# Performance work log

Measured on AMD Instinct MI355X. Metric: run time of the kernel, lower is better.

## Reference

```python
import jax, jax.numpy as jnp
import numpy as np

HEAD_DIM = 128
NUM_Q_HEADS = 16
NUM_KV_HEADS = 8
EPS = 1e-6


def _rope_tables(seq_len, head_dim, base=10000.0):
    inv_freq = 1.0 / (base ** (np.arange(0, head_dim, 2, dtype=np.float32) / head_dim))
    t = np.arange(seq_len, dtype=np.float32)
    freqs = np.outer(t, inv_freq)                      # [S, hd/2]
    emb = np.concatenate([freqs, freqs], axis=-1)      # [S, hd]
    return jnp.asarray(np.cos(emb)), jnp.asarray(np.sin(emb))


def setup_inputs() -> dict:
    key = jax.random.key(0)
    k1, k2, k3 = jax.random.split(key, 3)
    B, S, D = 2, 2048, 2048
    qo_dim = NUM_Q_HEADS * HEAD_DIM
    kv_dim = NUM_KV_HEADS * HEAD_DIM
    x = jax.random.normal(k1, (B, S, D), dtype=jnp.float32)
    w_qkv = jax.random.normal(k2, (qo_dim + 2 * kv_dim, D), dtype=jnp.float32) * 0.02
    w_o = jax.random.normal(k3, (D, qo_dim), dtype=jnp.float32) * 0.02
    pos_cos, pos_sin = _rope_tables(S, HEAD_DIM)
    return {
        "x": x,
        "pos_cos": pos_cos,
        "pos_sin": pos_sin,
        "w_qkv": w_qkv,
        "w_o": w_o,
        "q_norm_w": jnp.ones((HEAD_DIM,), dtype=jnp.float32),
        "k_norm_w": jnp.ones((HEAD_DIM,), dtype=jnp.float32),
    }


def _rms_norm(h, w):
    # per-head RMSNorm over last dim (head_dim)
    var = jnp.mean(jnp.square(h), axis=-1, keepdims=True)
    return h * jax.lax.rsqrt(var + EPS) * w


def _rotate_half(h):
    h1, h2 = jnp.split(h, 2, axis=-1)
    return jnp.concatenate([-h2, h1], axis=-1)


def _apply_rope(h, cos, sin):
    # h: [B, S, H, hd]; cos/sin: [S, hd]
    c = cos[None, :, None, :]
    s = sin[None, :, None, :]
    return h * c + _rotate_half(h) * s


def reference(x, pos_cos, pos_sin, w_qkv, w_o, q_norm_w, k_norm_w):
    B, S, D = x.shape
    hd = HEAD_DIM
    qkv = jnp.einsum("bsd,ed->bse", x, w_qkv).reshape(B, S, -1, hd)
    q = qkv[:, :, :NUM_Q_HEADS]                                   # [B,S,Hq,hd]
    k = qkv[:, :, NUM_Q_HEADS:NUM_Q_HEADS + NUM_KV_HEADS]         # [B,S,Hk,hd]
    v = qkv[:, :, NUM_Q_HEADS + NUM_KV_HEADS:]                    # [B,S,Hk,hd]

    q = _apply_rope(_rms_norm(q, q_norm_w), pos_cos, pos_sin)
    k = _apply_rope(_rms_norm(k, k_norm_w), pos_cos, pos_sin)

    # GQA: expand kv heads to match query heads
    rep = NUM_Q_HEADS // NUM_KV_HEADS
    k = jnp.repeat(k, rep, axis=2)
    v = jnp.repeat(v, rep, axis=2)

    scale = 1.0 / jnp.sqrt(jnp.float32(hd))
    scores = jnp.einsum("bqhd,bkhd->bhqk", q, k) * scale          # [B,H,S,S]
    causal = jnp.tril(jnp.ones((S, S), dtype=bool))
    scores = jnp.where(causal[None, None], scores, jnp.finfo(scores.dtype).min)
    attn = jax.nn.softmax(scores, axis=-1)
    out = jnp.einsum("bhqk,bkhd->bqhd", attn, v)                  # [B,S,H,hd]
    out = out.reshape(B, S, NUM_Q_HEADS * hd)
    return jnp.einsum("bse,de->bsd", out, w_o)
```

## Files before the change

### kernel.cpp

```cpp
#include <hip/hip_runtime.h>
#include <hip/hip_bf16.h>
#include <stdint.h>

#define HD 128
#define NQH 16
#define NKVH 8
#define SEQ 2048
#define DMODEL 2048
#define BATCH 2

typedef __attribute__((ext_vector_type(8))) short bf16x8;
typedef __attribute__((ext_vector_type(4))) float f32x4;
typedef __attribute__((ext_vector_type(16))) float f32x16;

__device__ __forceinline__ ushort f2bf(float f){
  union { float f; uint32_t u; } v; v.f = f;
  uint32_t u = v.u;
  return (ushort)((u + 0x7FFFu + ((u >> 16) & 1u)) >> 16);
}
__device__ __forceinline__ float bf2f(ushort h){
  union { uint32_t u; float f; } v; v.u = ((uint32_t)h) << 16; return v.f;
}
__device__ __forceinline__ void gload16(const void* g, void* l){
  __builtin_amdgcn_global_load_lds((const __attribute__((address_space(1))) void*)g,
                                   (__attribute__((address_space(3))) void*)l, 16, 0, 0);
}
__device__ __forceinline__ unsigned int cvtpk(float lo, float hi){
  unsigned int r;
  asm("v_cvt_pk_bf16_f32 %0, %1, %2" : "=v"(r) : "v"(lo), "v"(hi));
  return r;
}

__global__ void cvtbf(const float* __restrict__ in, ushort* __restrict__ out, int n4){
  int i = blockIdx.x * 256 + threadIdx.x;
  if (i < n4){
    float4 v = ((const float4*)in)[i];
    ushort4 o;
    o.x = f2bf(v.x); o.y = f2bf(v.y); o.z = f2bf(v.z); o.w = f2bf(v.w);
    ((ushort4*)out)[i] = o;
  }
}

template<int OUTF32>
__global__ __launch_bounds__(256) void gemm_bt(const ushort* __restrict__ A,
                                               const ushort* __restrict__ B,
                                               void* __restrict__ C,
                                               int M, int N, int K){
  __shared__ __align__(16) ushort lA[128*64];
  __shared__ __align__(16) ushort lB[128*64];
  const int tid = threadIdx.x;
  const int l = tid & 63, w = tid >> 6;
  const int m0 = blockIdx.y * 128, n0 = blockIdx.x * 128;
  const int wr = (w >> 1) * 64, wc = (w & 1) * 64;
  f32x4 acc[4][4];
  #pragma unroll
  for (int m=0;m<4;m++)
    #pragma unroll
    for (int n=0;n<4;n++) acc[m][n] = f32x4{0.f,0.f,0.f,0.f};

  const int srow = l >> 3;
  const int scol = ((l & 7) ^ srow) << 3;
  const ushort* gA = A + (size_t)(m0 + w*32 + srow) * K + scol;
  const ushort* gB = B + (size_t)(n0 + w*32 + srow) * K + scol;
  ushort* lAw = &lA[(w*32) * 64];
  ushort* lBw = &lB[(w*32) * 64];

  for (int kt = 0; kt < K; kt += 64){
    __syncthreads();
    #pragma unroll
    for (int j=0;j<4;j++){
      gload16(gA + kt + (size_t)(j*8)*K, lAw + j*8*64);
      gload16(gB + kt + (size_t)(j*8)*K, lBw + j*8*64);
    }
    __syncthreads();
    #pragma unroll
    for (int kk=0; kk<2; kk++){
      bf16x8 af[4], bb[4];
      #pragma unroll
      for (int m=0;m<4;m++){
        int row = wr + m*16 + (l & 15);
        int slot = (kk*4 + (l >> 4)) ^ (row & 7);
        af[m] = *(const bf16x8*)&lA[row*64 + slot*8];
      }
      #pragma unroll
      for (int n=0;n<4;n++){
        int row = wc + n*16 + (l & 15);
        int slot = (kk*4 + (l >> 4)) ^ (row & 7);
        bb[n] = *(const bf16x8*)&lB[row*64 + slot*8];
      }
      #pragma unroll
      for (int m=0;m<4;m++)
        #pragma unroll
        for (int n=0;n<4;n++)
          acc[m][n] = __builtin_amdgcn_mfma_f32_16x16x32_bf16(af[m], bb[n], acc[m][n], 0,0,0);
    }
  }
  #pragma unroll
  for (int m=0;m<4;m++)
    #pragma unroll
    for (int n=0;n<4;n++)
      #pragma unroll
      for (int r=0;r<4;r++){
        size_t row = (size_t)(m0 + wr + m*16 + (l>>4)*4 + r);
        size_t col = (size_t)(n0 + wc + n*16 + (l & 15));
        float v = acc[m][n][r];
        if (OUTF32) ((float*)C)[row*N + col] = v;
        else        ((ushort*)C)[row*N + col] = f2bf(v);
      }
}

__global__ __launch_bounds__(512, 1) void gemm256_bt(const ushort* __restrict__ A,
                                                     const ushort* __restrict__ B,
                                                     ushort* __restrict__ C,
                                                     int M, int N, int K){
  __shared__ __align__(16) ushort lA[2][256*64];
  __shared__ __align__(16) ushort lB[2][256*64];
  const int tid = threadIdx.x;
  const int l = tid & 63, w = tid >> 6;
  const int wm = w >> 2, wn = w & 3;
  const int m0 = blockIdx.y * 256, n0 = blockIdx.x * 256;
  const int NT = K >> 6;

  const int srow = w*8 + (l >> 3);
  const int scol = ((l & 7) ^ (l >> 3)) << 3;

  f32x4 acc[8][4];
  #pragma unroll
  for (int m=0;m<8;m++)
    #pragma unroll
    for (int n=0;n<4;n++) acc[m][n] = f32x4{0.f,0.f,0.f,0.f};

  auto stgA = [&](int t, int h){
    const int bi = t & 1;
    #pragma unroll
    for (int j=0;j<2;j++)
      gload16(A + (size_t)(m0 + h*128 + j*64 + srow)*K + t*64 + scol,
              &lA[bi][(h*128 + j*64 + w*8)*64]);
  };
  auto stgB = [&](int t, int h){
    const int bi = t & 1;
    #pragma unroll
    for (int j=0;j<2;j++)
      gload16(B + (size_t)(n0 + h*128 + j*64 + srow)*K + t*64 + scol,
              &lB[bi][(h*128 + j*64 + w*8)*64]);
  };

  stgA(0,0); stgA(0,1); stgB(0,0); stgB(0,1);
  stgA(1,0); stgB(1,0); stgB(1,1);
  asm volatile("s_waitcnt vmcnt(6)" ::: "memory");
  __builtin_amdgcn_s_barrier();

  for (int t=0; t<NT; t++){
    const int bi = t & 1;
    bf16x8 bfr[4][2];
    #pragma unroll
    for (int q=0; q<4; q++){
      bf16x8 af[2][2];
      #pragma unroll
      for (int mi2=0; mi2<2; mi2++)
        #pragma unroll
        for (int ks=0; ks<2; ks++){
          int row = wm*128 + (q*2 + mi2)*16 + (l & 15);
          int slot = (ks*4 + (l >> 4)) ^ (l & 7);
          af[mi2][ks] = *(const bf16x8*)&lA[bi][row*64 + slot*8];
        }
      if (q == 0){
        #pragma unroll
        for (int ni=0; ni<4; ni++)
          #pragma unroll
          for (int ks=0; ks<2; ks++){
            int row = wn*64 + ni*16 + (l & 15);
            int slot = (ks*4 + (l >> 4)) ^ (l & 7);
            bfr[ni][ks] = *(const bf16x8*)&lB[bi][row*64 + slot*8];
          }
      }
      if (q == 0 && t+1 < NT) stgA(t+1, 1);
      if (q == 1 && t+2 < NT) stgB(t+2, 0);
      if (q == 2 && t+2 < NT) stgB(t+2, 1);
      __builtin_amdgcn_s_barrier();
      asm volatile("s_waitcnt lgkmcnt(0)" ::: "memory");
      if (q == 3 && t+2 < NT) stgA(t+2, 0);
      __builtin_amdgcn_s_setprio(1);
      #pragma unroll
      for (int mi2=0; mi2<2; mi2++)
        #pragma unroll
        for (int ni=0; ni<4; ni++)
          #pragma unroll
          for (int ks=0; ks<2; ks++)
            acc[q*2+mi2][ni] = __builtin_amdgcn_mfma_f32_16x16x32_bf16(
                af[mi2][ks], bfr[ni][ks], acc[q*2+mi2][ni], 0,0,0);
      __builtin_amdgcn_s_setprio(0);
      if (q == 3){
        if (t < NT-2) { asm volatile("s_waitcnt vmcnt(6)" ::: "memory"); }
        else          { asm volatile("s_waitcnt vmcnt(0)" ::: "memory"); }
      }
      __builtin_amdgcn_s_barrier();
    }
  }

  #pragma unroll
  for (int mi=0; mi<8; mi++)
    #pragma unroll
    for (int ni=0; ni<4; ni++)
      #pragma unroll
      for (int r=0; r<4; r++){
        size_t row = (size_t)(m0 + wm*128 + mi*16 + (l>>4)*4 + r);
        size_t col = (size_t)(n0 + wn*64 + ni*16 + (l & 15));
        C[row*N + col] = f2bf(acc[mi][ni][r]);
      }
}

__global__ __launch_bounds__(256) void norm_rope(const ushort* __restrict__ qkv,
                                                 const float* __restrict__ cosT,
                                                 const float* __restrict__ sinT,
                                                 const float* __restrict__ qw,
                                                 const float* __restrict__ kw,
                                                 ushort* __restrict__ Qo,
                                                 ushort* __restrict__ Ko){
  int gw = (blockIdx.x * 256 + threadIdx.x) >> 6;
  int l = threadIdx.x & 63;
  int head = gw % 24;
  int bs = gw / 24;
  int s = bs & (SEQ-1);
  int b = bs >> 11;
  ushort2 hv = *(const ushort2*)(qkv + (size_t)bs*(2*DMODEL) + head*HD + l*2);
  float h0 = bf2f(hv.x), h1 = bf2f(hv.y);
  float ss = h0*h0 + h1*h1;
  #pragma unroll
  for (int m=1; m<64; m<<=1) ss += __shfl_xor(ss, m);
  float rinv = rsqrtf(ss * (1.0f/128.0f) + 1e-6f);
  const float* wp = (head < NQH) ? qw : kw;
  float w0 = wp[l*2], w1 = wp[l*2+1];
  float n0 = h0 * rinv * w0, n1 = h1 * rinv * w1;
  float p0 = __shfl_xor(n0, 32), p1 = __shfl_xor(n1, 32);
  float r0 = (l < 32) ? -p0 : p0;
  float r1 = (l < 32) ? -p1 : p1;
  float c0 = cosT[s*HD + l*2], c1 = cosT[s*HD + l*2 + 1];
  float s0 = sinT[s*HD + l*2], s1 = sinT[s*HD + l*2 + 1];
  float sc = (head < NQH) ? 0.12751656062f : 1.0f;
  ushort2 o;
  o.x = f2bf((n0*c0 + r0*s0) * sc);
  o.y = f2bf((n1*c1 + r1*s1) * sc);
  if (head < NQH)
    *(ushort2*)(Qo + ((size_t)((b*NQH + head)*SEQ) + s)*HD + l*2) = o;
  else
    *(ushort2*)(Ko + ((size_t)((b*NKVH + (head-NQH))*SEQ) + s)*HD + l*2) = o;
}

__global__ __launch_bounds__(256) void vtrans(const ushort* __restrict__ qkv, ushort* __restrict__ vt){
  __shared__ __align__(16) ushort t[64][136];
  int bid = blockIdx.x;
  int st = bid & 31, kh = (bid >> 5) & 7, b = bid >> 8;
  int s0 = st * 64;
  int tid = threadIdx.x;
  #pragma unroll
  for (int it=0; it<4; it++){
    int row = (tid >> 4) + it*16;
    int c = tid & 15;
    uint4 v = *(const uint4*)&qkv[((size_t)(b*SEQ + s0 + row))*(2*DMODEL) + (NQH+NKVH+kh)*HD + c*8];
    *(uint4*)&t[row][c*8] = v;
  }
  __syncthreads();
  #pragma unroll
  for (int it=0; it<4; it++){
    int g = it*256 + tid;
    int d = g >> 3, c = g & 7;
    ushort tmp[8] __attribute__((aligned(16)));
    #pragma unroll
    for (int j=0;j<8;j++) tmp[j] = t[c*8+j][d];
    *(uint4*)&vt[((size_t)((b*NKVH+kh)*HD + d))*SEQ + s0 + c*8] = *(uint4*)tmp;
  }
}

__global__ __launch_bounds__(256, 3) void attn_fwd(const ushort* __restrict__ Q,
                                                   const ushort* __restrict__ Kb,
                                                   const ushort* __restrict__ Vt,
                                                   ushort* __restrict__ O){
  __shared__ __align__(16) ushort lK[2][64*128];
  __shared__ __align__(16) ushort lV[128*64];
  const int l = threadIdx.x & 63, w = threadIdx.x >> 6;
  const int wq = w >> 1, wkv = w & 1;
  const int hl = l >> 5, q32 = l & 31;
  const int bid = blockIdx.x;
  const int qt = 31 - (bid >> 5);
  const int bh = bid & 31;
  const int head = bh & 15, b = bh >> 4;
  const int kh = head >> 1;

  const ushort* kg = Kb + (size_t)((b*NKVH + kh)*SEQ) * HD;
  const ushort* vg = Vt + (size_t)((b*NKVH + kh)*HD) * SEQ;

  auto STAGE_K = [&](int t, int bi){
    const int kv0 = t*64;
    #pragma unroll
    for (int j=0;j<4;j++){
      int krow = kv0 + w*16 + j*4 + (l>>4);
      gload16(kg + (size_t)krow*HD + (((l&15) ^ (krow&15))<<3),
              &lK[bi][(w*16 + j*4)*128]);
    }
  };
  auto STAGE_V = [&](int t){
    const int kv0 = t*64;
    #pragma unroll
    for (int j=0;j<4;j++){
      int vrow = w*32 + j*8 + (l>>3);
      gload16(vg + (size_t)vrow*SEQ + kv0 + (((l&7) ^ (l>>3))<<3),
              &lV[(w*32 + j*8)*64]);
    }
  };

  const int qb = qt*64 + wq*32;
  const ushort* qp = Q + ((size_t)((b*NQH + head)*SEQ) + qb + q32) * HD + hl*8;
  bf16x8 qf[8];
  #pragma unroll
  for (int ks=0; ks<8; ks++) qf[ks] = *(const bf16x8*)(qp + ks*16);

  float mrun = -1e30f, lrun = 0.f;
  f32x16 acc[4];
  #pragma unroll
  for (int dt=0;dt<4;dt++)
    #pragma unroll
    for (int r=0;r<16;r++) acc[dt][r] = 0.f;

  STAGE_K(0, 0);

  for (int t=0; t<=qt; t++){
    const int bi = t & 1;
    STAGE_V(t);
    STAGE_K(t < qt ? t+1 : qt, bi^1);
    asm volatile("s_waitcnt vmcnt(8)" ::: "memory");
    __builtin_amdgcn_s_barrier();

    const bool skip = (t==qt) && (wq==0) && (wkv==1);
    f32x16 s;
    if (!skip){
      #pragma unroll
      for (int r=0;r<16;r++) s[r] = 0.f;
      const int rowT = wkv*32 + q32;
      __builtin_amdgcn_s_setprio(1);
      #pragma unroll
      for (int ks=0; ks<8; ks++){
        int slot = (ks*2 + hl) ^ (rowT & 15);
        bf16x8 kf = *(const bf16x8*)&lK[bi][rowT*128 + slot*8];
        s = __builtin_amdgcn_mfma_f32_32x32x16_bf16(kf, qf[ks], s, 0,0,0);
      }
      __builtin_amdgcn_s_setprio(0);
      if (t==qt && wq==wkv){
        const int qg = qb + q32;
        #pragma unroll
        for (int r=0;r<16;r++){
          int kvg = t*64 + wkv*32 + (r&3) + 8*(r>>2) + 4*hl;
          s[r] = (kvg > qg) ? -1e30f : s[r];
        }
      }
      float t0 = fmaxf(fmaxf(s[0],s[1]),fmaxf(s[2],s[3]));
      float t1 = fmaxf(fmaxf(s[4],s[5]),fmaxf(s[6],s[7]));
      float t2 = fmaxf(fmaxf(s[8],s[9]),fmaxf(s[10],s[11]));
      float t3 = fmaxf(fmaxf(s[12],s[13]),fmaxf(s[14],s[15]));
      float tmax = fmaxf(fmaxf(t0,t1),fmaxf(t2,t3));
      tmax = fmaxf(tmax, __shfl_xor(tmax, 32));
      if (!__all(tmax <= mrun)){
        float mnew = fmaxf(mrun, tmax);
        float corr = __builtin_amdgcn_exp2f(mrun - mnew);
        mrun = mnew; lrun *= corr;
        #pragma unroll
        for (int r=0;r<16;r++){
          int qr = (r&3) + 8*(r>>2) + 4*hl;
          float cr = __shfl(corr, qr);
          acc[0][r]*=cr; acc[1][r]*=cr; acc[2][r]*=cr; acc[3][r]*=cr;
        }
      }
      #pragma unroll
      for (int r=0;r<16;r++) s[r] = __builtin_amdgcn_exp2f(s[r] - mrun);
      float r0s = (s[0]+s[1])+(s[2]+s[3]);
      float r1s = (s[4]+s[5])+(s[6]+s[7]);
      float r2s = (s[8]+s[9])+(s[10]+s[11]);
      float r3s = (s[12]+s[13])+(s[14]+s[15]);
      float rs = (r0s+r1s)+(r2s+r3s);
      rs += __shfl_xor(rs, 32);
      lrun += rs;
    }
    asm volatile("s_waitcnt vmcnt(4)" ::: "memory");
    __builtin_amdgcn_s_barrier();
    if (!skip){
      __builtin_amdgcn_s_setprio(1);
      #pragma unroll
      for (int ks2=0; ks2<2; ks2++){
        unsigned int A = cvtpk(s[8*ks2+0], s[8*ks2+1]);
        unsigned int B = cvtpk(s[8*ks2+2], s[8*ks2+3]);
        unsigned int C = cvtpk(s[8*ks2+4], s[8*ks2+5]);
        unsigned int D = cvtpk(s[8*ks2+6], s[8*ks2+7]);
        auto sw0 = __builtin_amdgcn_permlane32_swap(A, C, false, false);
        auto sw1 = __builtin_amdgcn_permlane32_swap(B, D, false, false);
        union { unsigned int u[4]; bf16x8 v; } pw;
        pw.u[0]=sw0[0]; pw.u[1]=sw1[0]; pw.u[2]=sw0[1]; pw.u[3]=sw1[1];
        #pragma unroll
        for (int dt=0; dt<4; dt++){
          int d = dt*32 + q32;
          int slot = (wkv*4 + ks2*2 + hl) ^ (d & 7);
          bf16x8 vf = *(const bf16x8*)&lV[d*64 + slot*8];
          acc[dt] = __builtin_amdgcn_mfma_f32_32x32x16_bf16(pw.v, vf, acc[dt], 0,0,0);
        }
      }
      __builtin_amdgcn_s_setprio(0);
    }
    asm volatile("s_waitcnt lgkmcnt(0)" ::: "memory");
    __builtin_amdgcn_s_barrier();
  }

  asm volatile("s_waitcnt vmcnt(0)" ::: "memory");
  __builtin_amdgcn_s_barrier();

  float* mergeO = (float*)(&lK[0][0]) + wq*4096;
  float* mergeML = (float*)(&lV[0]);
  if (wkv == 1){
    #pragma unroll
    for (int dt=0; dt<4; dt++)
      #pragma unroll
      for (int rg=0; rg<4; rg++){
        f32x4 o = { acc[dt][rg*4+0], acc[dt][rg*4+1], acc[dt][rg*4+2], acc[dt][rg*4+3] };
        *(f32x4*)&mergeO[(dt*4+rg)*256 + l*4] = o;
      }
    if (l < 32){
      mergeML[wq*64 + l] = mrun;
      mergeML[wq*64 + 32 + l] = lrun;
    }
  }
  __syncthreads();
  if (wkv == 0){
    float m1 = mergeML[wq*64 + q32];
    float l1 = mergeML[wq*64 + 32 + q32];
    float mf = fmaxf(mrun, m1);
    float c0 = __builtin_amdgcn_exp2f(mrun - mf);
    float c1 = __builtin_amdgcn_exp2f(m1 - mf);
    float lt = lrun*c0 + l1*c1;
    float linv = 1.0f / lt;
    float f0 = c0 * linv, f1 = c1 * linv;
    float g0a[16], g1a[16];
    #pragma unroll
    for (int r=0;r<16;r++){
      int qr = (r&3) + 8*(r>>2) + 4*hl;
      g0a[r] = __shfl(f0, qr);
      g1a[r] = __shfl(f1, qr);
    }
    #pragma unroll
    for (int dt=0; dt<4; dt++)
      #pragma unroll
      for (int rg=0; rg<4; rg++){
        f32x4 o1 = *(const f32x4*)&mergeO[(dt*4+rg)*256 + l*4];
        #pragma unroll
        for (int j=0;j<4;j++){
          int r = rg*4 + j;
          int qr = (r&3) + 8*(r>>2) + 4*hl;
          float val = acc[dt][r]*g0a[r] + o1[j]*g1a[r];
          int orow = qt*64 + wq*32 + qr;
          O[((size_t)(b*SEQ) + orow)*DMODEL + head*HD + dt*32 + q32] = f2bf(val);
        }
      }
  }
}

extern "C" void kernel_launch(void* const* d_in, const int* in_sizes, int n_in,
                              void* d_out, int out_size, void* d_ws, size_t ws_size,
                              hipStream_t stream){
  const float* x    = (const float*)d_in[0];
  const float* pcos = (const float*)d_in[1];
  const float* psin = (const float*)d_in[2];
  const float* wqkv = (const float*)d_in[3];
  const float* wo   = (const float*)d_in[4];
  const float* qnw  = (const float*)d_in[5];
  const float* knw  = (const float*)d_in[6];
  char* ws = (char*)d_ws;

  ushort* xb    = (ushort*)(ws + 0);
  ushort* wqkvb = (ushort*)(ws + 16777216);
  ushort* wob   = (ushort*)(ws + 33554432);
  ushort* qkv   = (ushort*)(ws + 41943040);
  ushort* qbuf  = (ushort*)(ws + 75497472);
  ushort* kbuf  = (ushort*)(ws + 92274688);
  ushort* vtb   = (ushort*)(ws + 100663296);
  ushort* aout  = (ushort*)(ws + 0);

  cvtbf<<<8192, 256, 0, stream>>>(x,    xb,    2097152);
  cvtbf<<<8192, 256, 0, stream>>>(wqkv, wqkvb, 2097152);
  cvtbf<<<4096, 256, 0, stream>>>(wo,   wob,   1048576);

  gemm256_bt<<<dim3(16,16), 512, 0, stream>>>(xb, wqkvb, qkv, 4096, 4096, 2048);

  norm_rope<<<24576, 256, 0, stream>>>(qkv, pcos, psin, qnw, knw, qbuf, kbuf);
  vtrans<<<512, 256, 0, stream>>>(qkv, vtb);

  attn_fwd<<<dim3(1024), 256, 0, stream>>>(qbuf, kbuf, vtb, aout);

  gemm_bt<1><<<dim3(16,32), 256, 0, stream>>>(aout, wob, d_out, 4096, 2048, 2048);
}
```

Baseline: 228.2 us.

## Split attention work across waves by query rows instead of KV halves

Each workgroup now handles a 128-row query tile, with each of the four waves owning 32 query rows and processing the full 64-wide KV tile. The earlier scheme split a 64-row query tile across two waves per KV half. This drops the cross-wave LDS merge of partial softmax states and halves the grid to 512 blocks, so each loaded K/V tile serves twice as many queries. The cost is more causal-imbalance work per block, with waves idling when fully masked, and fewer blocks for occupancy.

After: 287.9 us. +26.1%, slower.

```diff
diff --git a/kernel.cpp b/kernel.cpp
--- a/kernel.cpp
+++ b/kernel.cpp
@@ -279,13 +279,15 @@
   __shared__ __align__(16) ushort lK[2][64*128];
   __shared__ __align__(16) ushort lV[128*64];
   const int l = threadIdx.x & 63, w = threadIdx.x >> 6;
-  const int wq = w >> 1, wkv = w & 1;
   const int hl = l >> 5, q32 = l & 31;
   const int bid = blockIdx.x;
-  const int qt = 31 - (bid >> 5);
+  const int qt = 15 - (bid >> 5);
   const int bh = bid & 31;
   const int head = bh & 15, b = bh >> 4;
   const int kh = head >> 1;
+  const int nt = 2*qt + 2;
+  const int qw0 = qt*128 + w*32;
+  const int qg = qw0 + q32;
 
   const ushort* kg = Kb + (size_t)((b*NKVH + kh)*SEQ) * HD;
   const ushort* vg = Vt + (size_t)((b*NKVH + kh)*HD) * SEQ;
@@ -309,8 +311,9 @@
     }
   };
 
-  const int qb = qt*64 + wq*32;
-  const ushort* qp = Q + ((size_t)((b*NQH + head)*SEQ) + qb + q32) * HD + hl*8;
+  STAGE_K(0, 0);
+
+  const ushort* qp = Q + ((size_t)((b*NQH + head)*SEQ) + qw0 + q32) * HD + hl*8;
   bf16x8 qf[8];
   #pragma unroll
   for (int ks=0; ks<8; ks++) qf[ks] = *(const bf16x8*)(qp + ks*16);
@@ -322,42 +325,56 @@
     #pragma unroll
     for (int r=0;r<16;r++) acc[dt][r] = 0.f;
 
-  STAGE_K(0, 0);
-
-  for (int t=0; t<=qt; t++){
+  for (int t=0; t<nt; t++){
     const int bi = t & 1;
+    const int kv0 = t*64;
     STAGE_V(t);
-    STAGE_K(t < qt ? t+1 : qt, bi^1);
-    asm volatile("s_waitcnt vmcnt(8)" ::: "memory");
+    if (t < nt-1){
+      STAGE_K(t+1, bi^1);
+      asm volatile("s_waitcnt vmcnt(8)" ::: "memory");
+    } else {
+      asm volatile("s_waitcnt vmcnt(4)" ::: "memory");
+    }
     __builtin_amdgcn_s_barrier();
 
-    const bool skip = (t==qt) && (wq==0) && (wkv==1);
-    f32x16 s;
-    if (!skip){
-      #pragma unroll
-      for (int r=0;r<16;r++) s[r] = 0.f;
-      const int rowT = wkv*32 + q32;
+    const bool skipw = (kv0 > qw0 + 31);
+    const bool domask = !skipw && (kv0 + 63 > qw0);
+    f32x16 s2[2];
+    if (!skipw){
       __builtin_amdgcn_s_setprio(1);
       #pragma unroll
-      for (int ks=0; ks<8; ks++){
-        int slot = (ks*2 + hl) ^ (rowT & 15);
-        bf16x8 kf = *(const bf16x8*)&lK[bi][rowT*128 + slot*8];
-        s = __builtin_amdgcn_mfma_f32_32x32x16_bf16(kf, qf[ks], s, 0,0,0);
+      for (int kvh=0; kvh<2; kvh++){
+        f32x16 s;
+        #pragma unroll
+        for (int r=0;r<16;r++) s[r] = 0.f;
+        const int rowT = kvh*32 + q32;
+        #pragma unroll
+        for (int ks=0; ks<8; ks++){
+          int slot = (ks*2 + hl) ^ (rowT & 15);
+          bf16x8 kf = *(const bf16x8*)&lK[bi][rowT*128 + slot*8];
+          s = __builtin_amdgcn_mfma_f32_32x32x16_bf16(kf, qf[ks], s, 0,0,0);
+        }
+        s2[kvh] = s;
       }
       __builtin_amdgcn_s_setprio(0);
-      if (t==qt && wq==wkv){
-        const int qg = qb + q32;
-        #pragma unroll
-        for (int r=0;r<16;r++){
-          int kvg = t*64 + wkv*32 + (r&3) + 8*(r>>2) + 4*hl;
-          s[r] = (kvg > qg) ? -1e30f : s[r];
-        }
-      }
-      float t0 = fmaxf(fmaxf(s[0],s[1]),fmaxf(s[2],s[3]));
-      float t1 = fmaxf(fmaxf(s[4],s[5]),fmaxf(s[6],s[7]));
-      float t2 = fmaxf(fmaxf(s[8],s[9]),fmaxf(s[10],s[11]));
-      float t3 = fmaxf(fmaxf(s[12],s[13]),fmaxf(s[14],s[15]));
-      float tmax = fmaxf(fmaxf(t0,t1),fmaxf(t2,t3));
+      if (domask){
+        #pragma unroll
+        for (int kvh=0; kvh<2; kvh++)
+          #pragma unroll
+          for (int r=0;r<16;r++){
+            int kvg = kv0 + kvh*32 + (r&3) + 8*(r>>2) + 4*hl;
+            s2[kvh][r] = (kvg > qg) ? -1e30f : s2[kvh][r];
+          }
+      }
+      float tmax = -1e30f;
+      #pragma unroll
+      for (int kvh=0; kvh<2; kvh++){
+        float t0 = fmaxf(fmaxf(s2[kvh][0],s2[kvh][1]),fmaxf(s2[kvh][2],s2[kvh][3]));
+        float t1 = fmaxf(fmaxf(s2[kvh][4],s2[kvh][5]),fmaxf(s2[kvh][6],s2[kvh][7]));
+        float t2 = fmaxf(fmaxf(s2[kvh][8],s2[kvh][9]),fmaxf(s2[kvh][10],s2[kvh][11]));
+        float t3 = fmaxf(fmaxf(s2[kvh][12],s2[kvh][13]),fmaxf(s2[kvh][14],s2[kvh][15]));
+        tmax = fmaxf(tmax, fmaxf(fmaxf(t0,t1),fmaxf(t2,t3)));
+      }
       tmax = fmaxf(tmax, __shfl_xor(tmax, 32));
       if (!__all(tmax <= mrun)){
         float mnew = fmaxf(mrun, tmax);
@@ -370,26 +387,34 @@
           acc[0][r]*=cr; acc[1][r]*=cr; acc[2][r]*=cr; acc[3][r]*=cr;
         }
       }
-      #pragma unroll
-      for (int r=0;r<16;r++) s[r] = __builtin_amdgcn_exp2f(s[r] - mrun);
-      float r0s = (s[0]+s[1])+(s[2]+s[3]);
-      float r1s = (s[4]+s[5])+(s[6]+s[7]);
-      float r2s = (s[8]+s[9])+(s[10]+s[11]);
-      float r3s = (s[12]+s[13])+(s[14]+s[15]);
-      float rs = (r0s+r1s)+(r2s+r3s);
+      float rs = 0.f;
+      #pragma unroll
+      for (int kvh=0; kvh<2; kvh++){
+        #pragma unroll
+        for (int r=0;r<16;r++) s2[kvh][r] = __builtin_amdgcn_exp2f(s2[kvh][r] - mrun);
+        float r0s = (s2[kvh][0]+s2[kvh][1])+(s2[kvh][2]+s2[kvh][3]);
+        float r1s = (s2[kvh][4]+s2[kvh][5])+(s2[kvh][6]+s2[kvh][7]);
+        float r2s = (s2[kvh][8]+s2[kvh][9])+(s2[kvh][10]+s2[kvh][11]);
+        float r3s = (s2[kvh][12]+s2[kvh][13])+(s2[kvh][14]+s2[kvh][15]);
+        rs += (r0s+r1s)+(r2s+r3s);
+      }
       rs += __shfl_xor(rs, 32);
       lrun += rs;
     }
-    asm volatile("s_waitcnt vmcnt(4)" ::: "memory");
+
+    if (t < nt-1){ asm volatile("s_waitcnt vmcnt(4)" ::: "memory"); }
+    else         { asm volatile("s_waitcnt vmcnt(0)" ::: "memory"); }
     __builtin_amdgcn_s_barrier();
-    if (!skip){
+
+    if (!skipw){
       __builtin_amdgcn_s_setprio(1);
       #pragma unroll
-      for (int ks2=0; ks2<2; ks2++){
-        unsigned int A = cvtpk(s[8*ks2+0], s[8*ks2+1]);
-        unsigned int B = cvtpk(s[8*ks2+2], s[8*ks2+3]);
-        unsigned int C = cvtpk(s[8*ks2+4], s[8*ks2+5]);
-        unsigned int D = cvtpk(s[8*ks2+6], s[8*ks2+7]);
+      for (int ks2=0; ks2<4; ks2++){
+        const int kvh = ks2 >> 1, kk = ks2 & 1;
+        unsigned int A = cvtpk(s2[kvh][8*kk+0], s2[kvh][8*kk+1]);
+        unsigned int B = cvtpk(s2[kvh][8*kk+2], s2[kvh][8*kk+3]);
+        unsigned int C = cvtpk(s2[kvh][8*kk+4], s2[kvh][8*kk+5]);
+        unsigned int D = cvtpk(s2[kvh][8*kk+6], s2[kvh][8*kk+7]);
         auto sw0 = __builtin_amdgcn_permlane32_swap(A, C, false, false);
         auto sw1 = __builtin_amdgcn_permlane32_swap(B, D, false, false);
         union { unsigned int u[4]; bf16x8 v; } pw;
@@ -397,7 +422,7 @@
         #pragma unroll
         for (int dt=0; dt<4; dt++){
           int d = dt*32 + q32;
-          int slot = (wkv*4 + ks2*2 + hl) ^ (d & 7);
+          int slot = (ks2*2 + hl) ^ (d & 7);
           bf16x8 vf = *(const bf16x8*)&lV[d*64 + slot*8];
           acc[dt] = __builtin_amdgcn_mfma_f32_32x32x16_bf16(pw.v, vf, acc[dt], 0,0,0);
         }
@@ -408,56 +433,21 @@
     __builtin_amdgcn_s_barrier();
   }
 
-  asm volatile("s_waitcnt vmcnt(0)" ::: "memory");
-  __builtin_amdgcn_s_barrier();
-
-  float* mergeO = (float*)(&lK[0][0]) + wq*4096;
-  float* mergeML = (float*)(&lV[0]);
-  if (wkv == 1){
-    #pragma unroll
-    for (int dt=0; dt<4; dt++)
-      #pragma unroll
-      for (int rg=0; rg<4; rg++){
-        f32x4 o = { acc[dt][rg*4+0], acc[dt][rg*4+1], acc[dt][rg*4+2], acc[dt][rg*4+3] };
-        *(f32x4*)&mergeO[(dt*4+rg)*256 + l*4] = o;
-      }
-    if (l < 32){
-      mergeML[wq*64 + l] = mrun;
-      mergeML[wq*64 + 32 + l] = lrun;
-    }
-  }
-  __syncthreads();
-  if (wkv == 0){
-    float m1 = mergeML[wq*64 + q32];
-    float l1 = mergeML[wq*64 + 32 + q32];
-    float mf = fmaxf(mrun, m1);
-    float c0 = __builtin_amdgcn_exp2f(mrun - mf);
-    float c1 = __builtin_amdgcn_exp2f(m1 - mf);
-    float lt = lrun*c0 + l1*c1;
-    float linv = 1.0f / lt;
-    float f0 = c0 * linv, f1 = c1 * linv;
-    float g0a[16], g1a[16];
+  float linv = 1.0f / lrun;
+  float lrinv[16];
+  #pragma unroll
+  for (int r=0;r<16;r++){
+    int qr = (r&3) + 8*(r>>2) + 4*hl;
+    lrinv[r] = __shfl(linv, qr);
+  }
+  #pragma unroll
+  for (int dt=0; dt<4; dt++)
     #pragma unroll
     for (int r=0;r<16;r++){
       int qr = (r&3) + 8*(r>>2) + 4*hl;
-      g0a[r] = __shfl(f0, qr);
-      g1a[r] = __shfl(f1, qr);
-    }
-    #pragma unroll
-    for (int dt=0; dt<4; dt++)
-      #pragma unroll
-      for (int rg=0; rg<4; rg++){
-        f32x4 o1 = *(const f32x4*)&mergeO[(dt*4+rg)*256 + l*4];
-        #pragma unroll
-        for (int j=0;j<4;j++){
-          int r = rg*4 + j;
-          int qr = (r&3) + 8*(r>>2) + 4*hl;
-          float val = acc[dt][r]*g0a[r] + o1[j]*g1a[r];
-          int orow = qt*64 + wq*32 + qr;
-          O[((size_t)(b*SEQ) + orow)*DMODEL + head*HD + dt*32 + q32] = f2bf(val);
-        }
-      }
-  }
+      int orow = qw0 + qr;
+      O[((size_t)(b*SEQ) + orow)*DMODEL + head*HD + dt*32 + q32] = f2bf(acc[dt][r] * lrinv[r]);
+    }
 }
 
 extern "C" void kernel_launch(void* const* d_in, const int* in_sizes, int n_in,
@@ -490,7 +480,7 @@
   norm_rope<<<24576, 256, 0, stream>>>(qkv, pcos, psin, qnw, knw, qbuf, kbuf);
   vtrans<<<512, 256, 0, stream>>>(qkv, vtb);
 
-  attn_fwd<<<dim3(1024), 256, 0, stream>>>(qbuf, kbuf, vtb, aout);
+  attn_fwd<<<dim3(512), 256, 0, stream>>>(qbuf, kbuf, vtb, aout);
 
   gemm_bt<1><<<dim3(16,32), 256, 0, stream>>>(aout, wob, d_out, 4096, 2048, 2048);
 }
```
